# Kernel tuning notes

Measured on AMD Instinct MI355X. Metric: run time of the kernel, lower is better.

## Reference

```python
import jax, jax.numpy as jnp
import numpy as np
from jax import lax

B, T, D = 4, 1024, 1024
H = 16
HD = D // H
MIN_K, MAX_K = 3, 9
KS = (3, 5, 7, 9)  # candidate odd kernel sizes


def setup_inputs() -> dict:
    key = jax.random.key(0)
    ks = jax.random.split(key, 16)
    s = 0.02
    inp = {
        "x": jax.random.normal(ks[0], (B, T, D), jnp.float32),
        "Wq": jax.random.normal(ks[1], (D, D), jnp.float32) * s,
        "bq": jnp.zeros((D,), jnp.float32),
        "Wk": jax.random.normal(ks[2], (D, D), jnp.float32) * s,
        "bk": jnp.zeros((D,), jnp.float32),
        "Wv": jax.random.normal(ks[3], (D, D), jnp.float32) * s,
        "bv": jnp.zeros((D,), jnp.float32),
        # per-head Conv1d weights (H, out_ch=HD, in_ch=HD, MAX_K) and biases (H, HD)
        "conv_w": jax.random.normal(ks[4], (H, HD, HD, MAX_K), jnp.float32) * s,
        "conv_b": jax.random.normal(ks[5], (H, HD), jnp.float32) * s,
        # kernel_proj: Linear(1,16) -> ReLU -> Linear(16,1), stored as (in,out)
        "kp_w1": jax.random.normal(ks[6], (1, 16), jnp.float32) * 0.5,
        "kp_b1": jnp.zeros((16,), jnp.float32),
        "kp_w2": jax.random.normal(ks[7], (16, 1), jnp.float32) * 0.5,
        "kp_b2": jnp.zeros((1,), jnp.float32),
        "fc_w": jax.random.normal(ks[8], (D, D), jnp.float32) * s,
        "fc_b": jnp.zeros((D,), jnp.float32),
        "ln_g": jnp.ones((D,), jnp.float32),
        "ln_b": jnp.zeros((D,), jnp.float32),
    }
    return inp


def reference(x, Wq, bq, Wk, bk, Wv, bv, conv_w, conv_b,
              kp_w1, kp_b1, kp_w2, kp_b2, fc_w, fc_b, ln_g, ln_b):
    scale = HD ** -0.5
    q = (x @ Wq + bq).reshape(B, T, H, HD).transpose(0, 2, 1, 3)  # (B,H,T,HD)
    k = (x @ Wk + bk).reshape(B, T, H, HD).transpose(0, 2, 1, 3)
    v = (x @ Wv + bv).reshape(B, T, H, HD).transpose(0, 2, 1, 3)

    attn = jax.nn.softmax(jnp.einsum('bhqd,bhkd->bhqk', q, k) * scale, axis=-1)

    # head importance -> dynamic kernel size per head
    importance = attn.mean(axis=(-2, -1)).mean(axis=0)  # (H,)
    imp_norm = (importance - importance.min()) / (importance.max() - importance.min() + 1e-6)
    hmid = jax.nn.relu(imp_norm[:, None] @ kp_w1 + kp_b1)  # (H,16)
    frac = jax.nn.sigmoid((hmid @ kp_w2 + kp_b2)[:, 0])    # (H,)
    kv = jnp.round(MIN_K + frac * (MAX_K - MIN_K)).astype(jnp.int32)
    kv = kv + (1 - kv % 2)                                 # force odd
    kv = jnp.clip(kv, MIN_K, MAX_K)
    k_idx = jnp.clip((kv - MIN_K) // 2, 0, len(KS) - 1)    # (H,) candidate index

    out = jnp.einsum('bhqk,bhkd->bhqd', attn, v)           # (B,H,T,HD)
    out_c = out.transpose(0, 1, 3, 2).reshape(B, H * HD, T)  # NCH grouped layout

    center = MAX_K // 2
    cands = []
    for kk in KS:
        half = kk // 2
        w = conv_w[:, :, :, center - half:center + half + 1].reshape(H * HD, HD, kk)
        y = lax.conv_general_dilated(out_c, w, (1,), 'VALID',
                                     dimension_numbers=('NCH', 'OIH', 'NCH'),
                                     feature_group_count=H)
        y = y + conv_b.reshape(1, H * HD, 1)
        # smart edge-replication pad of conv OUTPUT back to length T
        y = jnp.pad(y, ((0, 0), (0, 0), (half, kk - 1 - half)), mode='edge')
        cands.append(y)
    cands = jnp.stack(cands).reshape(len(KS), B, H, HD, T)  # (K,B,H,HD,T)

    onehot = jax.nn.one_hot(k_idx, len(KS), dtype=cands.dtype)  # (H,K)
    sel = jnp.einsum('kbhdt,hk->bhdt', cands, onehot)           # (B,H,HD,T)
    out_cat = sel.transpose(0, 3, 1, 2).reshape(B, T, D)

    proj = out_cat @ fc_w + fc_b
    y = proj + x
    mu = y.mean(axis=-1, keepdims=True)
    var = ((y - mu) ** 2).mean(axis=-1, keepdims=True)
    return (y - mu) / jnp.sqrt(var + 1e-5) * ln_g + ln_b
```

## Files before the change

### kernel.cpp

```cpp
#include <hip/hip_runtime.h>
#include <math.h>

constexpr int Bn = 4, Tn = 1024, Dn = 1024, Hn = 16, HDn = 64;

typedef __attribute__((ext_vector_type(8))) short short8;
typedef __attribute__((ext_vector_type(4))) float floatx4;
typedef __attribute__((ext_vector_type(4))) unsigned short ushort4v;

static __device__ __forceinline__ unsigned short f2bf(float f) {
  union { float f; unsigned int u; } v; v.f = f;
  unsigned int u = v.u;
  unsigned int r = (u + 0x7fffu + ((u >> 16) & 1u)) >> 16;
  return (unsigned short)r;
}

static __device__ __forceinline__ unsigned short f2bf_fast(float f) {
  union { float f; unsigned int u; } v; v.f = f;
  return (unsigned short)((v.u + 0x8000u) >> 16);
}

static __device__ __forceinline__ void gload_lds16(const void* g, void* l) {
  __builtin_amdgcn_global_load_lds(
      (const __attribute__((address_space(1))) unsigned int*)g,
      (__attribute__((address_space(3))) unsigned int*)l, 16, 0, 0);
}


__global__ __launch_bounds__(256) void prep_misc(
    const float* __restrict__ X, unsigned short* __restrict__ Xb,
    const float* __restrict__ conv_w, unsigned short* __restrict__ Wc)
{
  if (blockIdx.x < 4096) {
    int i = (blockIdx.x * 256 + threadIdx.x) * 4;
    float4 v = *(const float4*)(X + i);
    ushort4v o;
    o.x = f2bf(v.x); o.y = f2bf(v.y); o.z = f2bf(v.z); o.w = f2bf(v.w);
    *(ushort4v*)(Xb + i) = o;
  } else {
    int idx = (blockIdx.x - 4096) * 256 + threadIdx.x;
    int i = idx & 63;
    int o = (idx >> 6) & 63;
    int j = (idx >> 12) % 7;
    int h = idx / (7 * 4096);
    Wc[idx] = f2bf(conv_w[(((size_t)(h * 64 + o) * 64 + i) * 9) + 1 + j]);
  }
}

__global__ __launch_bounds__(256) void transpose_cast(
    const float* __restrict__ W0, const float* __restrict__ W1,
    const float* __restrict__ W2, const float* __restrict__ W3,
    unsigned short* __restrict__ O0, unsigned short* __restrict__ O1,
    unsigned short* __restrict__ O2, unsigned short* __restrict__ O3)
{
  const int z = blockIdx.z;
  const float* W = (z == 0) ? W0 : (z == 1) ? W1 : (z == 2) ? W2 : W3;
  unsigned short* O = (z == 0) ? O0 : (z == 1) ? O1 : (z == 2) ? O2 : O3;
  __shared__ float tile[64][65];
  const int tid = threadIdx.x;
  const int c0 = blockIdx.x * 64, r0 = blockIdx.y * 64;
  for (int i = tid; i < 4096; i += 256) {
    int r = i >> 6, c = i & 63;
    tile[r][c] = W[(size_t)(r0 + r) * 1024 + c0 + c];
  }
  __syncthreads();
  for (int i = tid; i < 4096; i += 256) {
    int r = i >> 6, c = i & 63;
    O[(size_t)(c0 + r) * 1024 + r0 + c] = f2bf(tile[c][r]);
  }
}

__global__ __launch_bounds__(256) void gemm_qkv_mfma(
    const unsigned short* __restrict__ Ab,
    const unsigned short* __restrict__ WqT, const unsigned short* __restrict__ WkT,
    const unsigned short* __restrict__ WvT,
    const float* __restrict__ bq, const float* __restrict__ bk, const float* __restrict__ bv,
    unsigned short* __restrict__ Qb, unsigned short* __restrict__ Kb,
    unsigned short* __restrict__ Vtb)
{
  __shared__ unsigned short As[128 * 64];
  __shared__ unsigned short Bs[128 * 64];
  const int tid = threadIdx.x;
  const int lane = tid & 63;
  const int ln = lane & 15, g = lane >> 4;
  const int wave = tid >> 6;
  const int wm = (wave >> 1) * 64, wn = (wave & 1) * 64;
  const int m0 = blockIdx.y * 128;
  const int ng = blockIdx.x * 128;
  const int which = ng >> 10;
  const int n0 = ng & 1023;
  const unsigned short* Wt = (which == 0) ? WqT : (which == 1) ? WkT : WvT;
  const float* bia = (which == 0) ? bq : (which == 1) ? bk : bv;

  const unsigned short* aSrc[4]; unsigned short* aDst[4];
  const unsigned short* bSrc[4]; unsigned short* bDst[4];
  #pragma unroll
  for (int it = 0; it < 4; ++it) {
    int L = it * 256 + tid;
    int r = L >> 3, sc = L & 7;
    int c = sc ^ (r & 7);
    aSrc[it] = Ab + (size_t)(m0 + r) * 1024 + c * 8;
    aDst[it] = As + L * 8;
    bSrc[it] = Wt + (size_t)(n0 + r) * 1024 + c * 8;
    bDst[it] = Bs + L * 8;
  }

  floatx4 acc[4][4];
  #pragma unroll
  for (int mt = 0; mt < 4; ++mt)
    #pragma unroll
    for (int nt = 0; nt < 4; ++nt) acc[mt][nt] = (floatx4)0.f;

  for (int k0 = 0; k0 < 1024; k0 += 64) {
    __syncthreads();
    #pragma unroll
    for (int it = 0; it < 4; ++it) {
      gload_lds16(aSrc[it] + k0, aDst[it]);
      gload_lds16(bSrc[it] + k0, bDst[it]);
    }
    __syncthreads();
    #pragma unroll
    for (int s = 0; s < 2; ++s) {
      short8 af[4], bf[4];
      #pragma unroll
      for (int mt = 0; mt < 4; ++mt) {
        int R = wm + mt * 16 + ln;
        int ch = (s * 4 + g) ^ (R & 7);
        af[mt] = *(const short8*)&As[(R * 8 + ch) * 8];
      }
      #pragma unroll
      for (int nt = 0; nt < 4; ++nt) {
        int R = wn + nt * 16 + ln;
        int ch = (s * 4 + g) ^ (R & 7);
        bf[nt] = *(const short8*)&Bs[(R * 8 + ch) * 8];
      }
      #pragma unroll
      for (int mt = 0; mt < 4; ++mt)
        #pragma unroll
        for (int nt = 0; nt < 4; ++nt)
          acc[mt][nt] = __builtin_amdgcn_mfma_f32_16x16x32_bf16(af[mt], bf[nt], acc[mt][nt], 0, 0, 0);
    }
  }

  const int b = m0 >> 10;
  const int tbase = m0 & 1023;
  #pragma unroll
  for (int nt = 0; nt < 4; ++nt) {
    int nl = wn + nt * 16 + ln;
    float bv_ = bia[n0 + nl];
    int h = (n0 + nl) >> 6, hd = (n0 + nl) & 63;
    #pragma unroll
    for (int mt = 0; mt < 4; ++mt) {
      int t = tbase + wm + mt * 16 + g * 4;
      if (which < 2) {
        unsigned short* Out = (which == 0) ? Qb : Kb;
        size_t base = (((size_t)b * Hn + h) * Tn + t) * HDn + hd;
        #pragma unroll
        for (int r = 0; r < 4; ++r)
          Out[base + (size_t)r * HDn] = f2bf(acc[mt][nt][r] + bv_);
      } else {
        ushort4v o;
        #pragma unroll
        for (int r = 0; r < 4; ++r) o[r] = f2bf(acc[mt][nt][r] + bv_);
        *(ushort4v*)(Vtb + (((size_t)b * Hn + h) * HDn + hd) * Tn + t) = o;
      }
    }
  }
}

__global__ __launch_bounds__(256) void gemm_fc_mfma(
    const unsigned short* __restrict__ Ab, const unsigned short* __restrict__ WT,
    const float* __restrict__ bia, float* __restrict__ PR)
{
  __shared__ unsigned short As[128 * 64];
  __shared__ unsigned short Bs[128 * 64];
  const int tid = threadIdx.x;
  const int lane = tid & 63;
  const int ln = lane & 15, g = lane >> 4;
  const int wave = tid >> 6;
  const int wm = (wave >> 1) * 64, wn = (wave & 1) * 64;
  const int m0 = blockIdx.y * 128;
  const int n0 = blockIdx.x * 128;

  const unsigned short* aSrc[4]; unsigned short* aDst[4];
  const unsigned short* bSrc[4]; unsigned short* bDst[4];
  #pragma unroll
  for (int it = 0; it < 4; ++it) {
    int L = it * 256 + tid;
    int r = L >> 3, sc = L & 7;
    int c = sc ^ (r & 7);
    aSrc[it] = Ab + (size_t)(m0 + r) * 1024 + c * 8;
    aDst[it] = As + L * 8;
    bSrc[it] = WT + (size_t)(n0 + r) * 1024 + c * 8;
    bDst[it] = Bs + L * 8;
  }

  floatx4 acc[4][4];
  #pragma unroll
  for (int mt = 0; mt < 4; ++mt)
    #pragma unroll
    for (int nt = 0; nt < 4; ++nt) acc[mt][nt] = (floatx4)0.f;

  for (int k0 = 0; k0 < 1024; k0 += 64) {
    __syncthreads();
    #pragma unroll
    for (int it = 0; it < 4; ++it) {
      gload_lds16(aSrc[it] + k0, aDst[it]);
      gload_lds16(bSrc[it] + k0, bDst[it]);
    }
    __syncthreads();
    #pragma unroll
    for (int s = 0; s < 2; ++s) {
      short8 af[4], bf[4];
      #pragma unroll
      for (int mt = 0; mt < 4; ++mt) {
        int R = wm + mt * 16 + ln;
        int ch = (s * 4 + g) ^ (R & 7);
        af[mt] = *(const short8*)&As[(R * 8 + ch) * 8];
      }
      #pragma unroll
      for (int nt = 0; nt < 4; ++nt) {
        int R = wn + nt * 16 + ln;
        int ch = (s * 4 + g) ^ (R & 7);
        bf[nt] = *(const short8*)&Bs[(R * 8 + ch) * 8];
      }
      #pragma unroll
      for (int mt = 0; mt < 4; ++mt)
        #pragma unroll
        for (int nt = 0; nt < 4; ++nt)
          acc[mt][nt] = __builtin_amdgcn_mfma_f32_16x16x32_bf16(af[mt], bf[nt], acc[mt][nt], 0, 0, 0);
    }
  }

  #pragma unroll
  for (int nt = 0; nt < 4; ++nt) {
    int n = n0 + wn + nt * 16 + ln;
    float bv_ = bia[n];
    #pragma unroll
    for (int mt = 0; mt < 4; ++mt) {
      int m = m0 + wm + mt * 16 + g * 4;
      float* base = PR + (size_t)m * Dn + n;
      #pragma unroll
      for (int r = 0; r < 4; ++r) base[(size_t)r * Dn] = acc[mt][nt][r] + bv_;
    }
  }
}

__global__ __launch_bounds__(256) void attn_mfma(
    const unsigned short* __restrict__ Qb, const unsigned short* __restrict__ Kb,
    const unsigned short* __restrict__ Vtb, unsigned short* __restrict__ AO)
{
  __shared__ unsigned short Ks[64 * 64];
  __shared__ unsigned short Vts[64 * 64];
  __shared__ unsigned short Ps[64 * 72];

  const int bh = blockIdx.y;
  const int q0 = blockIdx.x * 64;
  const int tid = threadIdx.x;
  const int lane = tid & 63;
  const int ln = lane & 15;
  const int g  = lane >> 4;
  const int wq = (tid >> 6) * 16;

  const unsigned short* Kp  = Kb  + (size_t)bh * Tn * HDn;
  const unsigned short* Vtp = Vtb + (size_t)bh * HDn * Tn;

  const unsigned short* Qrow = Qb + ((size_t)bh * Tn + q0 + wq + ln) * HDn;
  short8 qa0 = *(const short8*)(Qrow + g * 8);
  short8 qa1 = *(const short8*)(Qrow + 32 + g * 8);

  const unsigned short* kSrc[2]; unsigned short* kDst[2];
  const unsigned short* vSrc[2]; unsigned short* vDst[2];
  #pragma unroll
  for (int it = 0; it < 2; ++it) {
    int L = it * 256 + tid;
    int r = L >> 3, sc = L & 7;
    int c = sc ^ (r & 7);
    kSrc[it] = Kp + (size_t)r * HDn + c * 8;
    kDst[it] = Ks + L * 8;
    vSrc[it] = Vtp + (size_t)r * Tn + c * 8;
    vDst[it] = Vts + L * 8;
  }

  floatx4 o[4];
  #pragma unroll
  for (int dt = 0; dt < 4; ++dt) o[dt] = (floatx4)0.f;
  float l[4] = {0.f, 0.f, 0.f, 0.f};

  constexpr float CEXP = 0.18033688011112042f;

  for (int kt = 0; kt < Tn; kt += 64) {
    __syncthreads();
    #pragma unroll
    for (int it = 0; it < 2; ++it) {
      gload_lds16(kSrc[it] + (size_t)kt * HDn, kDst[it]);
      gload_lds16(vSrc[it] + kt, vDst[it]);
    }
    __syncthreads();

    floatx4 s[4];
    #pragma unroll
    for (int nt = 0; nt < 4; ++nt) {
      int R = nt * 16 + ln;
      int ch0 = g ^ (ln & 7), ch1 = (4 + g) ^ (ln & 7);
      short8 kb0 = *(const short8*)&Ks[(R * 8 + ch0) * 8];
      short8 kb1 = *(const short8*)&Ks[(R * 8 + ch1) * 8];
      s[nt] = (floatx4)0.f;
      s[nt] = __builtin_amdgcn_mfma_f32_16x16x32_bf16(qa0, kb0, s[nt], 0, 0, 0);
      s[nt] = __builtin_amdgcn_mfma_f32_16x16x32_bf16(qa1, kb1, s[nt], 0, 0, 0);
    }

    #pragma unroll
    for (int r = 0; r < 4; ++r) {
      #pragma unroll
      for (int nt = 0; nt < 4; ++nt) {
        float pv = __builtin_amdgcn_exp2f(s[nt][r] * CEXP);
        l[r] += pv;
        Ps[(wq + g * 4 + r) * 72 + nt * 16 + ln] = f2bf_fast(pv);
      }
    }

    short8 pa0 = *(const short8*)&Ps[(wq + ln) * 72 + g * 8];
    short8 pa1 = *(const short8*)&Ps[(wq + ln) * 72 + 32 + g * 8];

    #pragma unroll
    for (int dt = 0; dt < 4; ++dt) {
      int R = dt * 16 + ln;
      int ch0 = g ^ (ln & 7), ch1 = (4 + g) ^ (ln & 7);
      short8 vb0 = *(const short8*)&Vts[(R * 8 + ch0) * 8];
      short8 vb1 = *(const short8*)&Vts[(R * 8 + ch1) * 8];
      o[dt] = __builtin_amdgcn_mfma_f32_16x16x32_bf16(pa0, vb0, o[dt], 0, 0, 0);
      o[dt] = __builtin_amdgcn_mfma_f32_16x16x32_bf16(pa1, vb1, o[dt], 0, 0, 0);
    }
  }

  float inv[4];
  #pragma unroll
  for (int r = 0; r < 4; ++r) {
    float rs = l[r];
    rs += __shfl_xor(rs, 1);
    rs += __shfl_xor(rs, 2);
    rs += __shfl_xor(rs, 4);
    rs += __shfl_xor(rs, 8);
    inv[r] = 1.f / rs;
  }
  unsigned short* Op = AO + ((size_t)bh * Tn + q0 + wq) * HDn;
  #pragma unroll
  for (int dt = 0; dt < 4; ++dt)
    #pragma unroll
    for (int r = 0; r < 4; ++r)
      Op[(size_t)(g * 4 + r) * HDn + dt * 16 + ln] = f2bf(o[dt][r] * inv[r]);
}

__global__ __launch_bounds__(256) void conv_mfma(
    const unsigned short* __restrict__ Xb, const unsigned short* __restrict__ Wc,
    const float* __restrict__ conv_b, unsigned short* __restrict__ CO)
{
  __shared__ unsigned short Wl[7 * 32 * 64];
  __shared__ unsigned short Xs[134 * 64];
  const int tid = threadIdx.x;
  const int lane = tid & 63;
  const int ln = lane & 15, g = lane >> 4;
  const int wave = tid >> 6;
  const int wm = wave * 32;
  const int t0 = blockIdx.x * 128;
  const int o0 = blockIdx.y * 32;
  const int bh = blockIdx.z;
  const int b = bh >> 4, h = bh & 15;
  const unsigned short* Xp = Xb + (size_t)bh * Tn * HDn;
  const unsigned short* Wp = Wc + ((size_t)h * 7 * 64 + o0) * 64;

  #pragma unroll
  for (int it = 0; it < 7; ++it) {
    int L = it * 256 + tid;
    int row = L >> 3, sc = L & 7;
    int c = sc ^ (row & 7);
    int j = row >> 5, ol = row & 31;
    gload_lds16(Wp + ((size_t)j * 64 + ol) * 64 + c * 8, Wl + L * 8);
  }
  #pragma unroll
  for (int it = 0; it < 5; ++it) {
    int L = it * 256 + tid;
    if (L < 134 * 8) {
      int lr = L >> 3, sc = L & 7;
      int c = sc ^ (lr & 7);
      int gr = min(max(t0 - 3 + lr, 0), Tn - 1);
      gload_lds16(Xp + (size_t)gr * HDn + c * 8, Xs + L * 8);
    }
  }
  __syncthreads();

  floatx4 acc[2][2];
  #pragma unroll
  for (int mt = 0; mt < 2; ++mt)
    #pragma unroll
    for (int nt = 0; nt < 2; ++nt) acc[mt][nt] = (floatx4)0.f;

  int tb[2];
  #pragma unroll
  for (int mt = 0; mt < 2; ++mt)
    tb[mt] = min(max(t0 + wm + mt * 16 + ln, 3), Tn - 4) - t0;

  #pragma unroll
  for (int j = 0; j < 7; ++j) {
    #pragma unroll
    for (int s = 0; s < 2; ++s) {
      short8 af[2], bf[2];
      #pragma unroll
      for (int mt = 0; mt < 2; ++mt) {
        int lr = tb[mt] + j;
        int ch = (s * 4 + g) ^ (lr & 7);
        af[mt] = *(const short8*)&Xs[lr * 64 + ch * 8];
      }
      #pragma unroll
      for (int nt = 0; nt < 2; ++nt) {
        int row = j * 32 + nt * 16 + ln;
        int ch = (s * 4 + g) ^ (row & 7);
        bf[nt] = *(const short8*)&Wl[row * 64 + ch * 8];
      }
      #pragma unroll
      for (int mt = 0; mt < 2; ++mt)
        #pragma unroll
        for (int nt = 0; nt < 2; ++nt)
          acc[mt][nt] = __builtin_amdgcn_mfma_f32_16x16x32_bf16(af[mt], bf[nt], acc[mt][nt], 0, 0, 0);
    }
  }

  #pragma unroll
  for (int nt = 0; nt < 2; ++nt) {
    int o = o0 + nt * 16 + ln;
    float bias = conv_b[(h << 6) + o];
    #pragma unroll
    for (int mt = 0; mt < 2; ++mt) {
      int t = t0 + wm + mt * 16 + g * 4;
      #pragma unroll
      for (int r = 0; r < 4; ++r)
        CO[((size_t)b * Tn + t + r) * Dn + (h << 6) + o] = f2bf(acc[mt][nt][r] + bias);
    }
  }
}

__global__ __launch_bounds__(256) void res_ln(
    const float* __restrict__ P, const float* __restrict__ Xin,
    const float* __restrict__ g, const float* __restrict__ be,
    float* __restrict__ Out)
{
  const int r = blockIdx.x;
  const int tid = threadIdx.x;
  const int c = tid * 4;
  float4 pv = *(const float4*)(P + (size_t)r * Dn + c);
  float4 xv = *(const float4*)(Xin + (size_t)r * Dn + c);
  float v0 = pv.x + xv.x, v1 = pv.y + xv.y, v2 = pv.z + xv.z, v3 = pv.w + xv.w;
  float s = v0 + v1 + v2 + v3;
  float s2 = v0 * v0 + v1 * v1 + v2 * v2 + v3 * v3;
  #pragma unroll
  for (int off = 32; off > 0; off >>= 1) {
    s += __shfl_down(s, off);
    s2 += __shfl_down(s2, off);
  }
  __shared__ float rs[4], rs2[4];
  __shared__ float smu, srstd;
  const int wid = tid >> 6;
  if ((tid & 63) == 0) { rs[wid] = s; rs2[wid] = s2; }
  __syncthreads();
  if (tid == 0) {
    float S = rs[0] + rs[1] + rs[2] + rs[3];
    float S2 = rs2[0] + rs2[1] + rs2[2] + rs2[3];
    float mu = S * (1.f / Dn);
    float var = S2 * (1.f / Dn) - mu * mu;
    smu = mu;
    srstd = rsqrtf(var + 1e-5f);
  }
  __syncthreads();
  float mu = smu, rstd = srstd;
  float4 gv = *(const float4*)(g + c);
  float4 bv = *(const float4*)(be + c);
  float4 ov;
  ov.x = (v0 - mu) * rstd * gv.x + bv.x;
  ov.y = (v1 - mu) * rstd * gv.y + bv.y;
  ov.z = (v2 - mu) * rstd * gv.z + bv.z;
  ov.w = (v3 - mu) * rstd * gv.w + bv.w;
  *(float4*)(Out + (size_t)r * Dn + c) = ov;
}

extern "C" void kernel_launch(void* const* d_in, const int* in_sizes, int n_in,
                              void* d_out, int out_size, void* d_ws, size_t ws_size,
                              hipStream_t stream) {
  const float* x      = (const float*)d_in[0];
  const float* Wq     = (const float*)d_in[1];
  const float* bq     = (const float*)d_in[2];
  const float* Wk     = (const float*)d_in[3];
  const float* bk     = (const float*)d_in[4];
  const float* Wv     = (const float*)d_in[5];
  const float* bv     = (const float*)d_in[6];
  const float* conv_w = (const float*)d_in[7];
  const float* conv_b = (const float*)d_in[8];
  const float* fc_w   = (const float*)d_in[13];
  const float* fc_b   = (const float*)d_in[14];
  const float* ln_g   = (const float*)d_in[15];
  const float* ln_b   = (const float*)d_in[16];
  float* out = (float*)d_out;

  unsigned char* w8 = (unsigned char*)d_ws;
  const size_t MB = 1024 * 1024;
  unsigned short* Xb  = (unsigned short*)(w8);
  unsigned short* WqT = (unsigned short*)(w8 + 8 * MB);
  unsigned short* WkT = (unsigned short*)(w8 + 10 * MB);
  unsigned short* WvT = (unsigned short*)(w8 + 12 * MB);
  unsigned short* fcT = (unsigned short*)(w8 + 14 * MB);
  unsigned short* Qb  = (unsigned short*)(w8 + 16 * MB);
  unsigned short* Kb  = (unsigned short*)(w8 + 24 * MB);
  unsigned short* Vtb = (unsigned short*)(w8 + 32 * MB);
  unsigned short* AO  = (unsigned short*)(w8 + 40 * MB);
  unsigned short* Wc  = (unsigned short*)(w8 + 48 * MB);
  unsigned short* CO  = (unsigned short*)(w8);
  float* PR           = (float*)(w8 + 16 * MB);

  prep_misc<<<dim3(4096 + 1792), 256, 0, stream>>>(x, Xb, conv_w, Wc);
  transpose_cast<<<dim3(16, 16, 4), 256, 0, stream>>>(Wq, Wk, Wv, fc_w, WqT, WkT, WvT, fcT);
  gemm_qkv_mfma<<<dim3(24, 32), 256, 0, stream>>>(Xb, WqT, WkT, WvT, bq, bk, bv, Qb, Kb, Vtb);
  attn_mfma<<<dim3(16, 64), 256, 0, stream>>>(Qb, Kb, Vtb, AO);
  conv_mfma<<<dim3(8, 2, 64), 256, 0, stream>>>(AO, Wc, conv_b, CO);
  gemm_fc_mfma<<<dim3(8, 32), 256, 0, stream>>>(CO, fcT, fc_b, PR);
  res_ln<<<dim3(Bn * Tn), 256, 0, stream>>>(PR, x, ln_g, ln_b, out);
}
```

Measured before the change: 231.5 us.

## Load GEMM MFMA fragments directly from global memory, dropping LDS staging

Both the QKV and FC GEMM kernels stop staging A/B tiles through shared memory with global_load_lds and two barriers per k-step. Each wave now loads its own MFMA fragments straight from global memory into registers, with a 2x unrolled k loop. This removes the barriers and LDS traffic, but operands shared between waves are no longer reused through LDS, so each A and B fragment is fetched twice per block and the kernels lean on the L1/L2 caches.

After: 323.9 us. +39.9%, slower.

```diff
diff --git a/kernel.cpp b/kernel.cpp
--- a/kernel.cpp
+++ b/kernel.cpp
@@ -77,8 +77,6 @@
     unsigned short* __restrict__ Qb, unsigned short* __restrict__ Kb,
     unsigned short* __restrict__ Vtb)
 {
-  __shared__ unsigned short As[128 * 64];
-  __shared__ unsigned short Bs[128 * 64];
   const int tid = threadIdx.x;
   const int lane = tid & 63;
   const int ln = lane & 15, g = lane >> 4;
@@ -91,18 +89,14 @@
   const unsigned short* Wt = (which == 0) ? WqT : (which == 1) ? WkT : WvT;
   const float* bia = (which == 0) ? bq : (which == 1) ? bk : bv;
 
-  const unsigned short* aSrc[4]; unsigned short* aDst[4];
-  const unsigned short* bSrc[4]; unsigned short* bDst[4];
-  #pragma unroll
-  for (int it = 0; it < 4; ++it) {
-    int L = it * 256 + tid;
-    int r = L >> 3, sc = L & 7;
-    int c = sc ^ (r & 7);
-    aSrc[it] = Ab + (size_t)(m0 + r) * 1024 + c * 8;
-    aDst[it] = As + L * 8;
-    bSrc[it] = Wt + (size_t)(n0 + r) * 1024 + c * 8;
-    bDst[it] = Bs + L * 8;
-  }
+  const unsigned short* aP[4];
+  const unsigned short* bP[4];
+  #pragma unroll
+  for (int mt = 0; mt < 4; ++mt)
+    aP[mt] = Ab + (size_t)(m0 + wm + mt * 16 + ln) * 1024 + g * 8;
+  #pragma unroll
+  for (int nt = 0; nt < 4; ++nt)
+    bP[nt] = Wt + (size_t)(n0 + wn + nt * 16 + ln) * 1024 + g * 8;
 
   floatx4 acc[4][4];
   #pragma unroll
@@ -110,35 +104,18 @@
     #pragma unroll
     for (int nt = 0; nt < 4; ++nt) acc[mt][nt] = (floatx4)0.f;
 
-  for (int k0 = 0; k0 < 1024; k0 += 64) {
-    __syncthreads();
-    #pragma unroll
-    for (int it = 0; it < 4; ++it) {
-      gload_lds16(aSrc[it] + k0, aDst[it]);
-      gload_lds16(bSrc[it] + k0, bDst[it]);
-    }
-    __syncthreads();
-    #pragma unroll
-    for (int s = 0; s < 2; ++s) {
-      short8 af[4], bf[4];
-      #pragma unroll
-      for (int mt = 0; mt < 4; ++mt) {
-        int R = wm + mt * 16 + ln;
-        int ch = (s * 4 + g) ^ (R & 7);
-        af[mt] = *(const short8*)&As[(R * 8 + ch) * 8];
-      }
-      #pragma unroll
-      for (int nt = 0; nt < 4; ++nt) {
-        int R = wn + nt * 16 + ln;
-        int ch = (s * 4 + g) ^ (R & 7);
-        bf[nt] = *(const short8*)&Bs[(R * 8 + ch) * 8];
-      }
-      #pragma unroll
-      for (int mt = 0; mt < 4; ++mt)
-        #pragma unroll
-        for (int nt = 0; nt < 4; ++nt)
-          acc[mt][nt] = __builtin_amdgcn_mfma_f32_16x16x32_bf16(af[mt], bf[nt], acc[mt][nt], 0, 0, 0);
-    }
+  #pragma unroll 2
+  for (int k0 = 0; k0 < 1024; k0 += 32) {
+    short8 af[4], bf[4];
+    #pragma unroll
+    for (int mt = 0; mt < 4; ++mt) af[mt] = *(const short8*)(aP[mt] + k0);
+    #pragma unroll
+    for (int nt = 0; nt < 4; ++nt) bf[nt] = *(const short8*)(bP[nt] + k0);
+    #pragma unroll
+    for (int mt = 0; mt < 4; ++mt)
+      #pragma unroll
+      for (int nt = 0; nt < 4; ++nt)
+        acc[mt][nt] = __builtin_amdgcn_mfma_f32_16x16x32_bf16(af[mt], bf[nt], acc[mt][nt], 0, 0, 0);
   }
 
   const int b = m0 >> 10;
@@ -171,8 +148,6 @@
     const unsigned short* __restrict__ Ab, const unsigned short* __restrict__ WT,
     const float* __restrict__ bia, float* __restrict__ PR)
 {
-  __shared__ unsigned short As[128 * 64];
-  __shared__ unsigned short Bs[128 * 64];
   const int tid = threadIdx.x;
   const int lane = tid & 63;
   const int ln = lane & 15, g = lane >> 4;
@@ -181,18 +156,14 @@
   const int m0 = blockIdx.y * 128;
   const int n0 = blockIdx.x * 128;
 
-  const unsigned short* aSrc[4]; unsigned short* aDst[4];
-  const unsigned short* bSrc[4]; unsigned short* bDst[4];
-  #pragma unroll
-  for (int it = 0; it < 4; ++it) {
-    int L = it * 256 + tid;
-    int r = L >> 3, sc = L & 7;
-    int c = sc ^ (r & 7);
-    aSrc[it] = Ab + (size_t)(m0 + r) * 1024 + c * 8;
-    aDst[it] = As + L * 8;
-    bSrc[it] = WT + (size_t)(n0 + r) * 1024 + c * 8;
-    bDst[it] = Bs + L * 8;
-  }
+  const unsigned short* aP[4];
+  const unsigned short* bP[4];
+  #pragma unroll
+  for (int mt = 0; mt < 4; ++mt)
+    aP[mt] = Ab + (size_t)(m0 + wm + mt * 16 + ln) * 1024 + g * 8;
+  #pragma unroll
+  for (int nt = 0; nt < 4; ++nt)
+    bP[nt] = WT + (size_t)(n0 + wn + nt * 16 + ln) * 1024 + g * 8;
 
   floatx4 acc[4][4];
   #pragma unroll
@@ -200,35 +171,18 @@
     #pragma unroll
     for (int nt = 0; nt < 4; ++nt) acc[mt][nt] = (floatx4)0.f;
 
-  for (int k0 = 0; k0 < 1024; k0 += 64) {
-    __syncthreads();
-    #pragma unroll
-    for (int it = 0; it < 4; ++it) {
-      gload_lds16(aSrc[it] + k0, aDst[it]);
-      gload_lds16(bSrc[it] + k0, bDst[it]);
-    }
-    __syncthreads();
-    #pragma unroll
-    for (int s = 0; s < 2; ++s) {
-      short8 af[4], bf[4];
-      #pragma unroll
-      for (int mt = 0; mt < 4; ++mt) {
-        int R = wm + mt * 16 + ln;
-        int ch = (s * 4 + g) ^ (R & 7);
-        af[mt] = *(const short8*)&As[(R * 8 + ch) * 8];
-      }
-      #pragma unroll
-      for (int nt = 0; nt < 4; ++nt) {
-        int R = wn + nt * 16 + ln;
-        int ch = (s * 4 + g) ^ (R & 7);
-        bf[nt] = *(const short8*)&Bs[(R * 8 + ch) * 8];
-      }
-      #pragma unroll
-      for (int mt = 0; mt < 4; ++mt)
-        #pragma unroll
-        for (int nt = 0; nt < 4; ++nt)
-          acc[mt][nt] = __builtin_amdgcn_mfma_f32_16x16x32_bf16(af[mt], bf[nt], acc[mt][nt], 0, 0, 0);
-    }
+  #pragma unroll 2
+  for (int k0 = 0; k0 < 1024; k0 += 32) {
+    short8 af[4], bf[4];
+    #pragma unroll
+    for (int mt = 0; mt < 4; ++mt) af[mt] = *(const short8*)(aP[mt] + k0);
+    #pragma unroll
+    for (int nt = 0; nt < 4; ++nt) bf[nt] = *(const short8*)(bP[nt] + k0);
+    #pragma unroll
+    for (int mt = 0; mt < 4; ++mt)
+      #pragma unroll
+      for (int nt = 0; nt < 4; ++nt)
+        acc[mt][nt] = __builtin_amdgcn_mfma_f32_16x16x32_bf16(af[mt], bf[nt], acc[mt][nt], 0, 0, 0);
   }
 
   #pragma unroll
```
